# Optimization experiments

Hardware: AMD Instinct MI355X
Metric: run time of the kernel (lower is better)

## Reference

```python
import jax, jax.numpy as jnp
import numpy as np
from jax import lax

ALPHA = 0.95
THRESH = 1.0
DN = ('NCDHW', 'OIDHW', 'NCDHW')  # (batch, chan, T, H, W)


def lif(x):
    # x: [B, C, T, H, W]. y[t] = (1-a)*y_reset[t-1] + x[t]; s = (y>=th); y *= (1-s)
    xt = jnp.moveaxis(x, 2, 0)  # [T, B, C, H, W]

    def step(y, x_t):
        y = (1.0 - ALPHA) * y + x_t
        s = (y >= THRESH).astype(x.dtype)
        return y * (1.0 - s), s

    _, s = lax.scan(step, jnp.zeros_like(xt[0]), xt)
    return jnp.moveaxis(s, 0, 2)  # back to [B, C, T, H, W]


def delta_encode(x):
    # temporal difference along T (axis 2), zero-padded at t=0
    d = x[:, :, 1:] - x[:, :, :-1]
    return jnp.concatenate([jnp.zeros_like(x[:, :, :1]), d], axis=2)


def setup_inputs() -> dict:
    key = jax.random.key(0)
    ks = jax.random.split(key, 7)
    B, H, W, T = 2, 64, 64, 350
    return {
        'x': jax.random.uniform(ks[0], (B, 2, H, W, T), dtype=jnp.float32),
        'conv1_w': jax.random.normal(ks[1], (8, 2, 5, 5, 1), dtype=jnp.float32) * 0.1,
        'conv1_b': jax.random.normal(ks[2], (8,), dtype=jnp.float32) * 0.1,
        'deconv_w': jax.random.normal(ks[3], (2, 8, 2, 2, 1), dtype=jnp.float32) * 0.1,
        'deconv_b': jax.random.normal(ks[4], (2,), dtype=jnp.float32) * 0.1,
        'conv2_w': jax.random.normal(ks[5], (2, 2), dtype=jnp.float32) * 0.1,
        'conv2_b': jax.random.normal(ks[6], (2,), dtype=jnp.float32) * 0.1,
    }


def reference(x, conv1_w, conv1_b, deconv_w, deconv_b, conv2_w, conv2_b):
    # x: [B, 2, H, W, T] -> [B, 2, T, H, W]
    h = jnp.transpose(x, (0, 1, 4, 2, 3))
    # conv1: kernel (5,5,1) over (T,H,W), padding (2,2,0)
    h = lax.conv_general_dilated(h, conv1_w, (1, 1, 1),
                                 [(2, 2), (2, 2), (0, 0)],
                                 dimension_numbers=DN)
    h = jax.nn.relu(h + conv1_b[None, :, None, None, None])
    h = lif(h)
    h = delta_encode(h)
    # deconv: kernel (2,2,1), stride (2,2,1) -> upsamples T and H by 2
    h = lax.conv_transpose(h, deconv_w, (2, 2, 1), 'VALID',
                           dimension_numbers=DN)
    h = h + deconv_b[None, :, None, None, None]
    # dropout3d(0.1) is identity in eval mode
    h = jax.nn.relu(h)
    # conv2: 1x1x1 conv == channel-mixing matmul
    h = jnp.einsum('oc,bcthw->bothw', conv2_w, h) + conv2_b[None, :, None, None, None]
    h = lif(h)
    # [B, C, T', H', W'] -> [B, C, H', W', T']
    return jnp.transpose(h, (0, 1, 3, 4, 2))
```

## Files before the change

### kernel.cpp

```cpp
#include <hip/hip_runtime.h>

constexpr int B  = 2,  CIN = 2,  H = 64, W = 64, T = 350;
constexpr int C1 = 8;
constexpr int TO = 700, HO = 128, WO = 64;
constexpr int HW = H * W;

#define DEC 0.05000000074505806f

__global__ void __launch_bounds__(256) transpose_kernel(
    const float* __restrict__ x, float* __restrict__ xT) {
  __shared__ float tile[64][65];
  int bid   = blockIdx.x;
  int tTile = bid % 6;
  int slice = bid / 6;
  int h  = slice % H;
  int bc = slice / H;
  int t0 = tTile * 64;
  int tx = threadIdx.x & 63;
  int tz = threadIdx.x >> 6;

  const float* src = x + ((long)bc * H + h) * (long)(W * T);
#pragma unroll
  for (int i = 0; i < 16; ++i) {
    int w = tz * 16 + i;
    int t = t0 + tx;
    tile[w][tx] = (t < T) ? src[(long)w * T + t] : 0.0f;
  }
  __syncthreads();
  float* dst = xT + ((long)bc * T) * HW + h * 64;
#pragma unroll
  for (int i = 0; i < 16; ++i) {
    int tl = tz * 16 + i;
    int t  = t0 + tl;
    if (t < T) dst[(long)t * HW + tx] = tile[tx][tl];
  }
}

__device__ __forceinline__ void gload_lds16(const float* g, float* l) {
  __builtin_amdgcn_global_load_lds(
      (const __attribute__((address_space(1))) unsigned int*)g,
      (__attribute__((address_space(3))) unsigned int*)l, 16, 0, 0);
}

__global__ void __launch_bounds__(512) convlif_kernel(
    const float* __restrict__ xT, const float* __restrict__ w1,
    const float* __restrict__ b1, signed char* __restrict__ d8) {
  __shared__ float buf[2][128 * 64];
  __shared__ __align__(16) unsigned char st[10][1024];
  const int tid = threadIdx.x;
  const int bid = blockIdx.x;
  const int chunk = bid & 3;
  const int rest  = bid >> 2;
  const int h2 = rest & 31;
  const int b  = rest >> 5;
  const int h0 = h2 * 2;
  const int w  = tid & 63;
  const int hs = (tid >> 6) & 1;
  const int cp = tid >> 7;
  const int h  = h0 + hs;
  const int wid = tid >> 6;

  const int tstore = chunk * 90;
  const int ts     = chunk ? tstore - 15 : 0;
  const int te     = tstore + 90 < T ? tstore + 90 : T;
  const int nsup   = (te - ts + 9) / 10;

  float wt[2][2][5][5];
#pragma unroll
  for (int ci = 0; ci < 2; ++ci)
#pragma unroll
    for (int dh = 0; dh < 5; ++dh) {
      int hh = h + dh - 2;
      bool hv = (hh >= 0) && (hh < H);
#pragma unroll
      for (int dt = 0; dt < 5; ++dt) {
        wt[0][ci][dt][dh] = hv ? w1[(((cp*2+0) * 2 + ci) * 5 + dt) * 5 + dh] : 0.0f;
        wt[1][ci][dt][dh] = hv ? w1[(((cp*2+1) * 2 + ci) * 5 + dt) * 5 + dh] : 0.0f;
      }
    }
  float bias0 = b1[cp*2], bias1 = b1[cp*2+1];

  int cdesc[4];
#pragma unroll
  for (int i = 0; i < 4; ++i) {
    int r = (tid >> 4) + 32 * i;
    if (r > 119) r = 119;
    int j   = r / 12;
    int rem = r - j * 12;
    int ci  = rem / 6;
    int dhh = rem - ci * 6;
    int hh = h0 + dhh - 2;
    int hc = hh < 0 ? 0 : (hh > H - 1 ? H - 1 : hh);
    cdesc[i] = (((b * 2 + ci) * T) * HW + hc * 64 + (tid & 15) * 4) | (j << 27);
  }

#pragma unroll
  for (int i = 0; i < 4; ++i) {
    int tau = ts + 3 + (cdesc[i] >> 27);
    if (tau > T - 1) tau = T - 1;
    gload_lds16(xT + (long)(cdesc[i] & 0x07ffffff) + (long)tau * HW,
                &buf[0][(i * 32 + wid * 4) * 64]);
  }

  float win[2][5][5];
#pragma unroll
  for (int ci = 0; ci < 2; ++ci)
#pragma unroll
    for (int dh = 0; dh < 5; ++dh) {
      int hh = h + dh - 2;
      int hc = hh < 0 ? 0 : (hh > H - 1 ? H - 1 : hh);
      const float* bp = xT + ((long)((b * 2 + ci) * T)) * HW + hc * 64 + w;
      win[ci][dh][3] = (ts >= 2) ? bp[(long)(ts - 2) * HW] : 0.0f;
      win[ci][dh][4] = (ts >= 1) ? bp[(long)(ts - 1) * HW] : 0.0f;
      win[ci][dh][0] = bp[(long)(ts + 0) * HW];
      win[ci][dh][1] = bp[(long)(ts + 1) * HW];
      win[ci][dh][2] = bp[(long)(ts + 2) * HW];
    }

  asm volatile("s_waitcnt vmcnt(0)" ::: "memory");
  __builtin_amdgcn_s_barrier();
  asm volatile("" ::: "memory");

  signed char* const d8row = d8 + ((long)(b * T)) * (HW * C1) + h0 * 512;
  const int stw = ((hs * 64 + w) * 8 + cp * 2) >> 1;

  float y0 = 0.0f, y1 = 0.0f, sp0 = 0.0f, sp1 = 0.0f;
  for (int k = 0; k < nsup; ++k) {
    asm volatile("s_waitcnt lgkmcnt(0)" ::: "memory");
    __builtin_amdgcn_s_barrier();
    asm volatile("" ::: "memory");

    if (k > 0) {
      int tb = ts + 10 * (k - 1);
#pragma unroll
      for (int i = 0; i < 2; ++i) {
        int slot = tid + i * 512;
        if (slot < 640) {
          int u = slot >> 6;
          int c = (slot & 63) * 16;
          int t = tb + u;
          if (t >= tstore && t < te) {
            uint4 v = *reinterpret_cast<const uint4*>(&st[u][c]);
            *reinterpret_cast<uint4*>(d8row + (long)t * (HW * C1) + c) = v;
          }
        }
      }
    }

    if (k + 1 < nsup) {
      int bs = ts + 3 + 10 * (k + 1);
      float* nb = &buf[(k + 1) & 1][0];
#pragma unroll
      for (int i = 0; i < 4; ++i) {
        int tau = bs + (cdesc[i] >> 27);
        if (tau > T - 1) tau = T - 1;
        gload_lds16(xT + (long)(cdesc[i] & 0x07ffffff) + (long)tau * HW,
                    nb + (i * 32 + wid * 4) * 64);
      }
      asm volatile("s_waitcnt vmcnt(4)" ::: "memory");
    } else {
      asm volatile("s_waitcnt vmcnt(0)" ::: "memory");
    }
    asm volatile("s_waitcnt lgkmcnt(0)" ::: "memory");
    __builtin_amdgcn_s_barrier();
    asm volatile("" ::: "memory");

    float* lb = &buf[k & 1][0];
    {
      int bufstart = ts + 3 + 10 * k;
      int rz0 = (T - bufstart) * 12;
      if (rz0 < 120) {
        if (rz0 < 0) rz0 = 0;
        for (int r = rz0 + wid; r < 120; r += 8) lb[r * 64 + w] = 0.0f;
        asm volatile("s_waitcnt lgkmcnt(0)" ::: "memory");
        __builtin_amdgcn_s_barrier();
        asm volatile("" ::: "memory");
      }
    }

    const int t0s = ts + 10 * k;
    for (int jj = 0; jj < 2; ++jj) {
#pragma unroll
      for (int u = 0; u < 5; ++u) {
        const int j5 = jj * 5;
        int t = t0s + j5 + u;
        float a0q0 = 0.f, a0q1 = 0.f, a0q2 = 0.f, a0q3 = 0.f;
        float a1q0 = 0.f, a1q1 = 0.f, a1q2 = 0.f, a1q3 = 0.f;
#pragma unroll
        for (int ci = 0; ci < 2; ++ci)
#pragma unroll
          for (int dt = 0; dt < 5; ++dt) {
            const int slot = (u + dt + 3) % 5;
#pragma unroll
            for (int dh = 0; dh < 5; ++dh) {
              const int q = (ci * 25 + dt * 5 + dh) & 3;
              float tap = win[ci][dh][slot];
              float p0 = tap * wt[0][ci][dt][dh];
              float p1 = tap * wt[1][ci][dt][dh];
              if (q == 0)      { a0q0 += p0; a1q0 += p1; }
              else if (q == 1) { a0q1 += p0; a1q1 += p1; }
              else if (q == 2) { a0q2 += p0; a1q2 += p1; }
              else             { a0q3 += p0; a1q3 += p1; }
            }
          }
        float a0 = fmaxf(((a0q0 + a0q1) + (a0q2 + a0q3)) + bias0, 0.0f);
        float a1 = fmaxf(((a1q0 + a1q1) + (a1q2 + a1q3)) + bias1, 0.0f);
        y0 = fmaf(DEC, y0, a0);
        y1 = fmaf(DEC, y1, a1);
        float s0 = (y0 >= 1.0f) ? 1.0f : 0.0f;
        float s1 = (y1 >= 1.0f) ? 1.0f : 0.0f;
        int d0 = (int)(s0 - sp0) & 0xff;
        int d1 = (int)(s1 - sp1) & 0xff;
        unsigned short val = (unsigned short)(d0 | (d1 << 8));
        if (t == 0) val = 0;
        reinterpret_cast<unsigned short*>(&st[j5 + u][0])[stw] = val;
        sp0 = s0; sp1 = s1;
        y0 = (s0 != 0.0f) ? 0.0f : y0;
        y1 = (s1 != 0.0f) ? 0.0f : y1;
        const int slot2 = (u + 3) % 5;
#pragma unroll
        for (int ci = 0; ci < 2; ++ci)
#pragma unroll
          for (int dh = 0; dh < 5; ++dh)
            win[ci][dh][slot2] =
                lb[((j5 + u) * 12 + ci * 6 + dh + hs) * 64 + w];
      }
    }
  }

  asm volatile("s_waitcnt lgkmcnt(0)" ::: "memory");
  __builtin_amdgcn_s_barrier();
  asm volatile("" ::: "memory");
  {
    int tb = ts + 10 * (nsup - 1);
#pragma unroll
    for (int i = 0; i < 2; ++i) {
      int slot = tid + i * 512;
      if (slot < 640) {
        int u = slot >> 6;
        int c = (slot & 63) * 16;
        int t = tb + u;
        if (t >= tstore && t < te) {
          uint4 v = *reinterpret_cast<const uint4*>(&st[u][c]);
          *reinterpret_cast<uint4*>(d8row + (long)t * (HW * C1) + c) = v;
        }
      }
    }
  }
}

__global__ void __launch_bounds__(64) stage2_kernel(
    const signed char* __restrict__ d8, const float* __restrict__ dw,
    const float* __restrict__ db, const float* __restrict__ cw,
    const float* __restrict__ cb, float* __restrict__ out) {
  __shared__ float SB[2][64][17];
  int bid   = blockIdx.x;
  int chunk = bid & 15;
  int rest  = bid >> 4;
  int hp = rest & 127;
  int b  = rest >> 7;
  int wp = threadIdx.x;

  int h  = hp >> 1;
  int kh = 1 - (hp & 1);

  float dwk0[2][8], dwk1[2][8];
#pragma unroll
  for (int c = 0; c < 2; ++c)
#pragma unroll
    for (int ci = 0; ci < 8; ++ci) {
      dwk0[c][ci] = dw[((c * 8 + ci) * 2 + 0) * 2 + kh];
      dwk1[c][ci] = dw[((c * 8 + ci) * 2 + 1) * 2 + kh];
    }
  float db0 = db[0], db1 = db[1];
  float cw00 = cw[0], cw01 = cw[1], cw10 = cw[2], cw11 = cw[3];
  float cb0 = cb[0], cb1 = cb[1];

  int t0 = chunk * 44;
  int t1 = (t0 + 44 < TO) ? t0 + 44 : TO;
  int tw = (t0 - 16 > 0) ? t0 - 16 : 0;

  const signed char* dbase = d8 + (((long)b * T) * HW + h * 64 + wp) * C1;
  const long tstride = (long)HW * C1;
  float* outb = out + ((long)b * 2 * HO) * (long)(WO * TO);

  float y0 = 0.0f, y1 = 0.0f;
  uint2 dc = *reinterpret_cast<const uint2*>(dbase + (long)(tw >> 1) * tstride);
  for (int tp = tw; tp < t1; tp += 2) {
    int tn = (tp + 2 < t1) ? ((tp + 2) >> 1) : ((t1 - 1) >> 1);
    uint2 dn = *reinterpret_cast<const uint2*>(dbase + (long)tn * tstride);

    float dv[8];
#pragma unroll
    for (int ci = 0; ci < 4; ++ci) {
      dv[ci]     = (float)(signed char)((dc.x >> (8 * ci)) & 0xff);
      dv[ci + 4] = (float)(signed char)((dc.y >> (8 * ci)) & 0xff);
    }

#pragma unroll
    for (int par = 0; par < 2; ++par) {
      int tpp = tp + par;
      float v0 = db0, v1 = db1;
      if (par == 0) {
#pragma unroll
        for (int ci = 0; ci < 8; ++ci) {
          v0 = fmaf(dv[ci], dwk1[0][ci], v0);
          v1 = fmaf(dv[ci], dwk1[1][ci], v1);
        }
      } else {
#pragma unroll
        for (int ci = 0; ci < 8; ++ci) {
          v0 = fmaf(dv[ci], dwk0[0][ci], v0);
          v1 = fmaf(dv[ci], dwk0[1][ci], v1);
        }
      }
      v0 = fmaxf(v0, 0.0f);
      v1 = fmaxf(v1, 0.0f);
      float u0 = fmaf(cw00, v0, fmaf(cw01, v1, cb0));
      float u1 = fmaf(cw10, v0, fmaf(cw11, v1, cb1));
      y0 = fmaf(DEC, y0, u0);
      y1 = fmaf(DEC, y1, u1);
      float s0 = (y0 >= 1.0f) ? 1.0f : 0.0f;
      float s1 = (y1 >= 1.0f) ? 1.0f : 0.0f;
      y0 = (s0 != 0.0f) ? 0.0f : y0;
      y1 = (s1 != 0.0f) ? 0.0f : y1;

      if (tpp >= t0) {
        int k = (tpp - t0) & 15;
        SB[0][wp][k] = s0;
        SB[1][wp][k] = s1;
        if (par == 1 && (k == 15 || tpp == t1 - 1)) {
          __syncthreads();
          int Kc  = k + 1;
          int t0f = tpp - k;
#pragma unroll
          for (int o = 0; o < 2; ++o) {
            float* ob = outb + ((long)(o * HO + hp)) * (long)(WO * TO);
#pragma unroll
            for (int i = 0; i < 4; ++i) {
              int idx = (i << 6) + wp;
              int r   = idx >> 2;
              int c   = (idx & 3) << 2;
              if (c < Kc) {
                float4 vv;
                vv.x = SB[o][r][c + 0];
                vv.y = SB[o][r][c + 1];
                vv.z = SB[o][r][c + 2];
                vv.w = SB[o][r][c + 3];
                *reinterpret_cast<float4*>(ob + (long)r * TO + (t0f + c)) = vv;
              }
            }
          }
          __syncthreads();
        }
      }
    }
    dc = dn;
  }
}

extern "C" void kernel_launch(void* const* d_in, const int* in_sizes, int n_in,
                              void* d_out, int out_size, void* d_ws, size_t ws_size,
                              hipStream_t stream) {
  const float* x  = (const float*)d_in[0];
  const float* w1 = (const float*)d_in[1];
  const float* b1 = (const float*)d_in[2];
  const float* dw = (const float*)d_in[3];
  const float* db = (const float*)d_in[4];
  const float* cw = (const float*)d_in[5];
  const float* cb = (const float*)d_in[6];
  float* out = (float*)d_out;

  float* xT = (float*)d_ws;
  signed char* d8 = (signed char*)d_ws + (size_t)B * CIN * T * HW * 4;

  transpose_kernel<<<dim3(B * CIN * H * 6), dim3(256), 0, stream>>>(x, xT);
  convlif_kernel<<<dim3(B * 32 * 4), dim3(512), 0, stream>>>(xT, w1, b1, d8);
  stage2_kernel<<<dim3(B * HO * 16), dim3(64), 0, stream>>>(d8, dw, db, cw, cb, out);
}
```

Measured before the change: 104.0 us.

## Fuse deconv/conv2/LIF stage into conv-LIF kernel via double-buffered LDS spikes

Drops the separate stage2 kernel and the global int8 delta buffer. The conv+LIF kernel now keeps each 10-step slab of delta spikes in a double-buffered LDS array, and the same block runs the deconv, conv2 and second LIF pass on the previous slab before computing the next. This removes a kernel launch and the global write and read of the intermediate. In exchange, each block does more serial work per step, and the warm-up overlap grows from 15 to 25 steps to cover the second LIF's state. Output stores become strided float2 writes per thread along T rather than coalesced tile stores.

Measured after the change: 108.9 us. +4.7%, slower.

```diff
diff --git a/kernel.cpp b/kernel.cpp
--- a/kernel.cpp
+++ b/kernel.cpp
@@ -6,6 +6,11 @@
 constexpr int HW = H * W;
 
 #define DEC 0.05000000074505806f
+
+__device__ __forceinline__ float rfl(float x) {
+  return __int_as_float(
+      __builtin_amdgcn_readfirstlane(__float_as_int(x)));
+}
 
 __global__ void __launch_bounds__(256) transpose_kernel(
     const float* __restrict__ x, float* __restrict__ xT) {
@@ -42,17 +47,18 @@
       (__attribute__((address_space(3))) unsigned int*)l, 16, 0, 0);
 }
 
-__global__ void __launch_bounds__(512) convlif_kernel(
+__global__ void __launch_bounds__(512) fused_kernel(
     const float* __restrict__ xT, const float* __restrict__ w1,
-    const float* __restrict__ b1, signed char* __restrict__ d8) {
+    const float* __restrict__ b1, const float* __restrict__ dwv,
+    const float* __restrict__ dbv, const float* __restrict__ cwv,
+    const float* __restrict__ cbv, float* __restrict__ out) {
   __shared__ float buf[2][128 * 64];
-  __shared__ __align__(16) unsigned char st[10][1024];
+  __shared__ __align__(8) unsigned char st[2][10][1024];
   const int tid = threadIdx.x;
   const int bid = blockIdx.x;
   const int chunk = bid & 3;
-  const int rest  = bid >> 2;
-  const int h2 = rest & 31;
-  const int b  = rest >> 5;
+  const int h2 = (bid >> 2) & 31;
+  const int b  = bid >> 7;
   const int h0 = h2 * 2;
   const int w  = tid & 63;
   const int hs = (tid >> 6) & 1;
@@ -61,7 +67,7 @@
   const int wid = tid >> 6;
 
   const int tstore = chunk * 90;
-  const int ts     = chunk ? tstore - 15 : 0;
+  const int ts     = chunk ? tstore - 25 : 0;
   const int te     = tstore + 90 < T ? tstore + 90 : T;
   const int nsup   = (te - ts + 9) / 10;
 
@@ -79,6 +85,24 @@
       }
     }
   float bias0 = b1[cp*2], bias1 = b1[cp*2+1];
+
+  const int hq = __builtin_amdgcn_readfirstlane(tid >> 7);
+  const int oo = __builtin_amdgcn_readfirstlane((tid >> 6) & 1);
+  const int hs2 = hq >> 1;
+  const int kh  = 1 - (hq & 1);
+  float dk0[2][8], dk1[2][8];
+#pragma unroll
+  for (int c = 0; c < 2; ++c)
+#pragma unroll
+    for (int ci = 0; ci < 8; ++ci) {
+      dk0[c][ci] = rfl(dwv[((c * 8 + ci) * 2 + 0) * 2 + kh]);
+      dk1[c][ci] = rfl(dwv[((c * 8 + ci) * 2 + 1) * 2 + kh]);
+    }
+  const float db0 = rfl(dbv[0]), db1 = rfl(dbv[1]);
+  const float cwa = rfl(cwv[oo * 2]), cwb = rfl(cwv[oo * 2 + 1]);
+  const float cbo = rfl(cbv[oo]);
+  float* const orow =
+      out + ((long)((b * 2 + oo) * HO + (h0 * 2 + hq)) * WO + w) * (long)TO;
 
   int cdesc[4];
 #pragma unroll
@@ -121,31 +145,58 @@
   __builtin_amdgcn_s_barrier();
   asm volatile("" ::: "memory");
 
-  signed char* const d8row = d8 + ((long)(b * T)) * (HW * C1) + h0 * 512;
-  const int stw = ((hs * 64 + w) * 8 + cp * 2) >> 1;
+  const int stw = (hs * 64 + w) * 4 + cp;
 
   float y0 = 0.0f, y1 = 0.0f, sp0 = 0.0f, sp1 = 0.0f;
+  float y2 = 0.0f;
+
+  auto lif2pass = [&](int kprev) {
+    const unsigned char* stp = &st[kprev & 1][0][0];
+    const int tb = ts + 10 * kprev;
+#pragma unroll
+    for (int u = 0; u < 10; ++u) {
+      int t = tb + u;
+      uint2 dvv = *reinterpret_cast<const uint2*>(
+          stp + u * 1024 + (hs2 * 64 + w) * 8);
+      float dv[8];
+#pragma unroll
+      for (int ci = 0; ci < 4; ++ci) {
+        dv[ci]     = (float)(signed char)((dvv.x >> (8 * ci)) & 0xff);
+        dv[ci + 4] = (float)(signed char)((dvv.y >> (8 * ci)) & 0xff);
+      }
+      float v0 = db0, v1 = db1;
+#pragma unroll
+      for (int ci = 0; ci < 8; ++ci) {
+        v0 = fmaf(dv[ci], dk1[0][ci], v0);
+        v1 = fmaf(dv[ci], dk1[1][ci], v1);
+      }
+      v0 = fmaxf(v0, 0.0f); v1 = fmaxf(v1, 0.0f);
+      float uo = fmaf(cwa, v0, fmaf(cwb, v1, cbo));
+      y2 = fmaf(DEC, y2, uo);
+      float s0 = (y2 >= 1.0f) ? 1.0f : 0.0f;
+      y2 = (s0 != 0.0f) ? 0.0f : y2;
+      v0 = db0; v1 = db1;
+#pragma unroll
+      for (int ci = 0; ci < 8; ++ci) {
+        v0 = fmaf(dv[ci], dk0[0][ci], v0);
+        v1 = fmaf(dv[ci], dk0[1][ci], v1);
+      }
+      v0 = fmaxf(v0, 0.0f); v1 = fmaxf(v1, 0.0f);
+      uo = fmaf(cwa, v0, fmaf(cwb, v1, cbo));
+      y2 = fmaf(DEC, y2, uo);
+      float s1 = (y2 >= 1.0f) ? 1.0f : 0.0f;
+      y2 = (s1 != 0.0f) ? 0.0f : y2;
+      if (t >= tstore && t < te) {
+        float2 vv; vv.x = s0; vv.y = s1;
+        *reinterpret_cast<float2*>(orow + 2 * t) = vv;
+      }
+    }
+  };
+
   for (int k = 0; k < nsup; ++k) {
     asm volatile("s_waitcnt lgkmcnt(0)" ::: "memory");
     __builtin_amdgcn_s_barrier();
     asm volatile("" ::: "memory");
-
-    if (k > 0) {
-      int tb = ts + 10 * (k - 1);
-#pragma unroll
-      for (int i = 0; i < 2; ++i) {
-        int slot = tid + i * 512;
-        if (slot < 640) {
-          int u = slot >> 6;
-          int c = (slot & 63) * 16;
-          int t = tb + u;
-          if (t >= tstore && t < te) {
-            uint4 v = *reinterpret_cast<const uint4*>(&st[u][c]);
-            *reinterpret_cast<uint4*>(d8row + (long)t * (HW * C1) + c) = v;
-          }
-        }
-      }
-    }
 
     if (k + 1 < nsup) {
       int bs = ts + 3 + 10 * (k + 1);
@@ -178,6 +229,9 @@
       }
     }
 
+    if (k > 0) lif2pass(k - 1);
+
+    unsigned short* stks = reinterpret_cast<unsigned short*>(&st[k & 1][0][0]);
     const int t0s = ts + 10 * k;
     for (int jj = 0; jj < 2; ++jj) {
 #pragma unroll
@@ -213,7 +267,7 @@
         int d1 = (int)(s1 - sp1) & 0xff;
         unsigned short val = (unsigned short)(d0 | (d1 << 8));
         if (t == 0) val = 0;
-        reinterpret_cast<unsigned short*>(&st[j5 + u][0])[stw] = val;
+        stks[(j5 + u) * 512 + stw] = val;
         sp0 = s0; sp1 = s1;
         y0 = (s0 != 0.0f) ? 0.0f : y0;
         y1 = (s1 != 0.0f) ? 0.0f : y1;
@@ -231,132 +285,7 @@
   asm volatile("s_waitcnt lgkmcnt(0)" ::: "memory");
   __builtin_amdgcn_s_barrier();
   asm volatile("" ::: "memory");
-  {
-    int tb = ts + 10 * (nsup - 1);
-#pragma unroll
-    for (int i = 0; i < 2; ++i) {
-      int slot = tid + i * 512;
-      if (slot < 640) {
-        int u = slot >> 6;
-        int c = (slot & 63) * 16;
-        int t = tb + u;
-        if (t >= tstore && t < te) {
-          uint4 v = *reinterpret_cast<const uint4*>(&st[u][c]);
-          *reinterpret_cast<uint4*>(d8row + (long)t * (HW * C1) + c) = v;
-        }
-      }
-    }
-  }
-}
-
-__global__ void __launch_bounds__(64) stage2_kernel(
-    const signed char* __restrict__ d8, const float* __restrict__ dw,
-    const float* __restrict__ db, const float* __restrict__ cw,
-    const float* __restrict__ cb, float* __restrict__ out) {
-  __shared__ float SB[2][64][17];
-  int bid   = blockIdx.x;
-  int chunk = bid & 15;
-  int rest  = bid >> 4;
-  int hp = rest & 127;
-  int b  = rest >> 7;
-  int wp = threadIdx.x;
-
-  int h  = hp >> 1;
-  int kh = 1 - (hp & 1);
-
-  float dwk0[2][8], dwk1[2][8];
-#pragma unroll
-  for (int c = 0; c < 2; ++c)
-#pragma unroll
-    for (int ci = 0; ci < 8; ++ci) {
-      dwk0[c][ci] = dw[((c * 8 + ci) * 2 + 0) * 2 + kh];
-      dwk1[c][ci] = dw[((c * 8 + ci) * 2 + 1) * 2 + kh];
-    }
-  float db0 = db[0], db1 = db[1];
-  float cw00 = cw[0], cw01 = cw[1], cw10 = cw[2], cw11 = cw[3];
-  float cb0 = cb[0], cb1 = cb[1];
-
-  int t0 = chunk * 44;
-  int t1 = (t0 + 44 < TO) ? t0 + 44 : TO;
-  int tw = (t0 - 16 > 0) ? t0 - 16 : 0;
-
-  const signed char* dbase = d8 + (((long)b * T) * HW + h * 64 + wp) * C1;
-  const long tstride = (long)HW * C1;
-  float* outb = out + ((long)b * 2 * HO) * (long)(WO * TO);
-
-  float y0 = 0.0f, y1 = 0.0f;
-  uint2 dc = *reinterpret_cast<const uint2*>(dbase + (long)(tw >> 1) * tstride);
-  for (int tp = tw; tp < t1; tp += 2) {
-    int tn = (tp + 2 < t1) ? ((tp + 2) >> 1) : ((t1 - 1) >> 1);
-    uint2 dn = *reinterpret_cast<const uint2*>(dbase + (long)tn * tstride);
-
-    float dv[8];
-#pragma unroll
-    for (int ci = 0; ci < 4; ++ci) {
-      dv[ci]     = (float)(signed char)((dc.x >> (8 * ci)) & 0xff);
-      dv[ci + 4] = (float)(signed char)((dc.y >> (8 * ci)) & 0xff);
-    }
-
-#pragma unroll
-    for (int par = 0; par < 2; ++par) {
-      int tpp = tp + par;
-      float v0 = db0, v1 = db1;
-      if (par == 0) {
-#pragma unroll
-        for (int ci = 0; ci < 8; ++ci) {
-          v0 = fmaf(dv[ci], dwk1[0][ci], v0);
-          v1 = fmaf(dv[ci], dwk1[1][ci], v1);
-        }
-      } else {
-#pragma unroll
-        for (int ci = 0; ci < 8; ++ci) {
-          v0 = fmaf(dv[ci], dwk0[0][ci], v0);
-          v1 = fmaf(dv[ci], dwk0[1][ci], v1);
-        }
-      }
-      v0 = fmaxf(v0, 0.0f);
-      v1 = fmaxf(v1, 0.0f);
-      float u0 = fmaf(cw00, v0, fmaf(cw01, v1, cb0));
-      float u1 = fmaf(cw10, v0, fmaf(cw11, v1, cb1));
-      y0 = fmaf(DEC, y0, u0);
-      y1 = fmaf(DEC, y1, u1);
-      float s0 = (y0 >= 1.0f) ? 1.0f : 0.0f;
-      float s1 = (y1 >= 1.0f) ? 1.0f : 0.0f;
-      y0 = (s0 != 0.0f) ? 0.0f : y0;
-      y1 = (s1 != 0.0f) ? 0.0f : y1;
-
-      if (tpp >= t0) {
-        int k = (tpp - t0) & 15;
-        SB[0][wp][k] = s0;
-        SB[1][wp][k] = s1;
-        if (par == 1 && (k == 15 || tpp == t1 - 1)) {
-          __syncthreads();
-          int Kc  = k + 1;
-          int t0f = tpp - k;
-#pragma unroll
-          for (int o = 0; o < 2; ++o) {
-            float* ob = outb + ((long)(o * HO + hp)) * (long)(WO * TO);
-#pragma unroll
-            for (int i = 0; i < 4; ++i) {
-              int idx = (i << 6) + wp;
-              int r   = idx >> 2;
-              int c   = (idx & 3) << 2;
-              if (c < Kc) {
-                float4 vv;
-                vv.x = SB[o][r][c + 0];
-                vv.y = SB[o][r][c + 1];
-                vv.z = SB[o][r][c + 2];
-                vv.w = SB[o][r][c + 3];
-                *reinterpret_cast<float4*>(ob + (long)r * TO + (t0f + c)) = vv;
-              }
-            }
-          }
-          __syncthreads();
-        }
-      }
-    }
-    dc = dn;
-  }
+  lif2pass(nsup - 1);
 }
 
 extern "C" void kernel_launch(void* const* d_in, const int* in_sizes, int n_in,
@@ -372,9 +301,8 @@
   float* out = (float*)d_out;
 
   float* xT = (float*)d_ws;
-  signed char* d8 = (signed char*)d_ws + (size_t)B * CIN * T * HW * 4;
 
   transpose_kernel<<<dim3(B * CIN * H * 6), dim3(256), 0, stream>>>(x, xT);
-  convlif_kernel<<<dim3(B * 32 * 4), dim3(512), 0, stream>>>(xT, w1, b1, d8);
-  stage2_kernel<<<dim3(B * HO * 16), dim3(64), 0, stream>>>(d8, dw, db, cw, cb, out);
-}
+  fused_kernel<<<dim3(B * 32 * 4), dim3(512), 0, stream>>>(
+      xT, w1, b1, dw, db, cw, cb, out);
+}
```
